# Optimization experiments

Hardware: AMD Instinct MI355X
Metric: run time of the kernel (lower is better)

Reference implementation:

```python
import jax, jax.numpy as jnp
import numpy as np

N = 50000
E = 800000
IN_DIM = 128
OUT_DIM = 128


def setup_inputs() -> dict:
    key = jax.random.key(0)
    k1, k2, k3, k4 = jax.random.split(key, 4)
    x = jax.random.normal(k1, (N, IN_DIM), dtype=jnp.float32)
    edge_index = jax.random.randint(k2, (2, E), 0, N, dtype=jnp.int64)
    # Linear(in_dim*2, out_dim) params
    W = jax.random.normal(k3, (2 * IN_DIM, OUT_DIM), dtype=jnp.float32) * (1.0 / np.sqrt(2 * IN_DIM))
    b = jax.random.normal(k4, (OUT_DIM,), dtype=jnp.float32) * 0.01
    return {"x": x, "edge_index": edge_index, "W": W, "b": b}


def reference(x, edge_index, W, b):
    src, dst = edge_index[0], edge_index[1]
    diff = x[src] - x[dst]                              # (E, C)
    # segment-max over destination nodes; empty segments get -inf identity
    seg_max = jax.ops.segment_max(diff, dst, num_segments=N)  # (N, C)
    counts = jax.ops.segment_sum(jnp.ones((E,), dtype=jnp.int32), dst, num_segments=N)
    # original code leaves zeros for nodes with no incoming edges
    max_diff = jnp.where((counts > 0)[:, None], seg_max, jnp.zeros_like(seg_max))
    x_cat = jnp.concatenate([x, max_diff], axis=-1)     # (N, 2C)
    return x_cat @ W + b
```

## Files before the change

kernel.cpp:

```cpp
#include <hip/hip_runtime.h>
#include <math.h>

#define NN 50000
#define NE 800000
#define CD 128
#define PB 3200
#define NBLK 1563
#define CSTR 1568
#define SCAP 160

typedef __attribute__((ext_vector_type(8))) short short8;
typedef __attribute__((ext_vector_type(4))) float f32x4;


__device__ inline unsigned pack2bf(float lo, float hi) {
    unsigned a = __float_as_uint(lo), b = __float_as_uint(hi);
    a = (a + 0x7fffu + ((a >> 16) & 1u)) >> 16;
    b = (b + 0x7fffu + ((b >> 16) & 1u)) & 0xffff0000u;
    return a | b;
}

__device__ inline unsigned short f2bf(float f) {
    unsigned u = __float_as_uint(f);
    return (unsigned short)((u + 0x7fffu + ((u >> 16) & 1u)) >> 16);
}

__device__ inline void fmax8(float* m, uint4 v) {
    m[0] = fmaxf(m[0], __uint_as_float(v.x << 16));
    m[1] = fmaxf(m[1], __uint_as_float(v.x & 0xffff0000u));
    m[2] = fmaxf(m[2], __uint_as_float(v.y << 16));
    m[3] = fmaxf(m[3], __uint_as_float(v.y & 0xffff0000u));
    m[4] = fmaxf(m[4], __uint_as_float(v.z << 16));
    m[5] = fmaxf(m[5], __uint_as_float(v.z & 0xffff0000u));
    m[6] = fmaxf(m[6], __uint_as_float(v.w << 16));
    m[7] = fmaxf(m[7], __uint_as_float(v.w & 0xffff0000u));
}


__global__ __launch_bounds__(256) void prep4_k(const int* __restrict__ ei,
                                               const float* __restrict__ x,
                                               const float* __restrict__ W,
                                               int* __restrict__ cur,
                                               int* __restrict__ ovfn,
                                               unsigned* __restrict__ ovf,
                                               unsigned* __restrict__ ent,
                                               unsigned* __restrict__ xb,
                                               unsigned short* __restrict__ wt) {
    int t = threadIdx.x;
    int b = blockIdx.x;
    int tid0 = b * 256 + t;
    int g = b & 7;
    int phase = (b >> 3) & 1;

    for (int p = 0; p < 2; p++) {
        if ((p ^ phase) == 0) {
            for (int e = tid0; e < NE; e += PB * 256) {
                int d = ei[NE + e];
                int s = ei[e];
                int bin = d >> 5;
                int pos = atomicAdd(&cur[g * CSTR + bin], 1);
                if (pos < SCAP) {
                    ent[(size_t)(g * NBLK + bin) * SCAP + pos] =
                        ((unsigned)s << 6) | (unsigned)(d & 31);
                } else {
                    int op = atomicAdd(ovfn, 1);
                    ovf[op] = ((unsigned)s << 16) | (unsigned)d;
                }
            }
        } else {
            for (int i = tid0; i < NN * CD / 4; i += PB * 256) {
                float4 v = ((const float4*)x)[i];
                uint2 r;
                r.x = pack2bf(v.x, v.y);
                r.y = pack2bf(v.z, v.w);
                ((uint2*)xb)[i] = r;
            }
        }
    }
    for (int i = tid0; i < 2 * CD * CD; i += PB * 256) {
        int n = i >> 8, k = i & 255;
        wt[(size_t)n * 256 + k] = f2bf(W[(size_t)k * 128 + n]);
    }
}


__global__ __launch_bounds__(256) void fused_k(const unsigned* __restrict__ xb,
                                               const int* __restrict__ cur,
                                               const int* __restrict__ ovfn,
                                               const unsigned* __restrict__ ovf,
                                               const unsigned* __restrict__ ent,
                                               const short* __restrict__ wt,
                                               const float* __restrict__ bias,
                                               float* __restrict__ out) {
    __shared__ unsigned short idx[32][72];
    __shared__ unsigned short amx[32][136];
    __shared__ int lcnt[32];
    __shared__ int spill[512];
    __shared__ int spn;

    int t = threadIdx.x;
    int b = blockIdx.x;
    int nbase = b * 32;

    if (t < 32) lcnt[t] = 0;
    if (t == 32) spn = 0;
    __syncthreads();

    for (int g = 0; g < 8; g++) {
        int cnt = min(cur[g * CSTR + b], SCAP);
        const unsigned* base = ent + (size_t)(g * NBLK + b) * SCAP;
        if (t < cnt) {
            unsigned w = base[t];
            int ln = (int)(w & 31u);
            int s = (int)(w >> 6);
            int pos = atomicAdd(&lcnt[ln], 1);
            if (pos < 64) idx[ln][pos] = (unsigned short)s;
            else { int sp = atomicAdd(&spn, 1); if (sp < 512) spill[sp] = (s << 6) | ln; }
        }
    }
    int ovN = min(ovfn[0], NE);
    for (int i = t; i < ovN; i += 256) {
        unsigned w = ovf[i];
        int d = (int)(w & 0xffffu);
        if ((d >> 5) == b) {
            int ln = d & 31;
            int s = (int)(w >> 16);
            int pos = atomicAdd(&lcnt[ln], 1);
            if (pos < 64) idx[ln][pos] = (unsigned short)s;
            else { int sp = atomicAdd(&spn, 1); if (sp < 512) spill[sp] = (s << 6) | ln; }
        }
    }
    __syncthreads();

    int w = t >> 6, lane = t & 63;
    int q = lane >> 4, c = lane & 15;
    int sN = min(spn, 512);
#pragma unroll 1
    for (int j = 0; j < 2; j++) {
        int ln = w * 8 + j * 4 + q;
        int node = nbase + ln;
        int cnt = lcnt[ln];
        int lim = min(cnt, 64);
        float m[8];
#pragma unroll
        for (int i = 0; i < 8; i++) m[i] = -INFINITY;

        for (int base = 0; base < lim; base += 8) {
            uint4 pk = *(const uint4*)&idx[ln][base];
            int s0 = (int)(pk.x & 0xffffu), s1 = (int)(pk.x >> 16);
            int s2 = (int)(pk.y & 0xffffu), s3 = (int)(pk.y >> 16);
            int s4 = (int)(pk.z & 0xffffu), s5 = (int)(pk.z >> 16);
            int s6 = (int)(pk.w & 0xffffu), s7 = (int)(pk.w >> 16);
            if (base + 8 <= lim) {
                fmax8(m, *(const uint4*)(xb + (size_t)s0 * 64 + c * 4));
                fmax8(m, *(const uint4*)(xb + (size_t)s1 * 64 + c * 4));
                fmax8(m, *(const uint4*)(xb + (size_t)s2 * 64 + c * 4));
                fmax8(m, *(const uint4*)(xb + (size_t)s3 * 64 + c * 4));
                fmax8(m, *(const uint4*)(xb + (size_t)s4 * 64 + c * 4));
                fmax8(m, *(const uint4*)(xb + (size_t)s5 * 64 + c * 4));
                fmax8(m, *(const uint4*)(xb + (size_t)s6 * 64 + c * 4));
                fmax8(m, *(const uint4*)(xb + (size_t)s7 * 64 + c * 4));
            } else {
                if (base + 0 < lim) fmax8(m, *(const uint4*)(xb + (size_t)s0 * 64 + c * 4));
                if (base + 1 < lim) fmax8(m, *(const uint4*)(xb + (size_t)s1 * 64 + c * 4));
                if (base + 2 < lim) fmax8(m, *(const uint4*)(xb + (size_t)s2 * 64 + c * 4));
                if (base + 3 < lim) fmax8(m, *(const uint4*)(xb + (size_t)s3 * 64 + c * 4));
                if (base + 4 < lim) fmax8(m, *(const uint4*)(xb + (size_t)s4 * 64 + c * 4));
                if (base + 5 < lim) fmax8(m, *(const uint4*)(xb + (size_t)s5 * 64 + c * 4));
                if (base + 6 < lim) fmax8(m, *(const uint4*)(xb + (size_t)s6 * 64 + c * 4));
                if (base + 7 < lim) fmax8(m, *(const uint4*)(xb + (size_t)s7 * 64 + c * 4));
            }
        }
        for (int i = 0; i < sN; i++) {
            int sw = spill[i];
            if ((sw & 63) == ln)
                fmax8(m, *(const uint4*)(xb + (size_t)(sw >> 6) * 64 + c * 4));
        }
        uint4 r = make_uint4(0u, 0u, 0u, 0u);
        if (cnt > 0) {
            uint4 xd = *(const uint4*)(xb + (size_t)node * 64 + c * 4);
            float d0 = m[0] - __uint_as_float(xd.x << 16);
            float d1 = m[1] - __uint_as_float(xd.x & 0xffff0000u);
            float d2 = m[2] - __uint_as_float(xd.y << 16);
            float d3 = m[3] - __uint_as_float(xd.y & 0xffff0000u);
            float d4 = m[4] - __uint_as_float(xd.z << 16);
            float d5 = m[5] - __uint_as_float(xd.z & 0xffff0000u);
            float d6 = m[6] - __uint_as_float(xd.w << 16);
            float d7 = m[7] - __uint_as_float(xd.w & 0xffff0000u);
            r.x = pack2bf(d0, d1);
            r.y = pack2bf(d2, d3);
            r.z = pack2bf(d4, d5);
            r.w = pack2bf(d6, d7);
        }
        *(uint4*)&amx[ln][c * 8] = r;
    }
    __syncthreads();

    int mm = lane & 15, g4 = lane >> 4;
    int rt = w & 1, ch = w >> 1;
    int r0 = nbase + rt * 16;
    int row = r0 + mm;
    bool rowok = row < NN;

    f32x4 acc[4];
#pragma unroll
    for (int ct = 0; ct < 4; ct++) {
        float bv = bias[ch * 64 + ct * 16 + mm];
        acc[ct] = (f32x4){bv, bv, bv, bv};
    }

    const short* xbs = (const short*)xb;
#pragma unroll
    for (int kc = 0; kc < 8; kc++) {
        int k0 = kc * 32;
        short8 a;
        if (kc < 4) {
            a = (short8){0, 0, 0, 0, 0, 0, 0, 0};
            if (rowok) a = *(const short8*)(xbs + (size_t)row * 128 + k0 + g4 * 8);
        } else {
            a = *(const short8*)&amx[rt * 16 + mm][(k0 - 128) + g4 * 8];
        }
#pragma unroll
        for (int ct = 0; ct < 4; ct++) {
            short8 bb = *(const short8*)(wt + (size_t)(ch * 64 + ct * 16 + mm) * 256 + k0 + g4 * 8);
            acc[ct] = __builtin_amdgcn_mfma_f32_16x16x32_bf16(a, bb, acc[ct], 0, 0, 0);
        }
    }

#pragma unroll
    for (int ct = 0; ct < 4; ct++) {
#pragma unroll
        for (int i = 0; i < 4; i++) {
            int rr = r0 + g4 * 4 + i;
            if (rr < NN) out[(size_t)rr * 128 + ch * 64 + ct * 16 + mm] = acc[ct][i];
        }
    }
}


extern "C" void kernel_launch(void* const* d_in, const int* in_sizes, int n_in,
                              void* d_out, int out_size, void* d_ws, size_t ws_size,
                              hipStream_t stream) {
    const float* x = (const float*)d_in[0];
    const int* ei = (const int*)d_in[1];
    const float* W = (const float*)d_in[2];
    const float* bias = (const float*)d_in[3];
    float* out = (float*)d_out;

    int* wsi = (int*)d_ws;
    int* cur   = wsi;
    int* ovfn  = wsi + 12544;
    unsigned* ovf = (unsigned*)(wsi + 12560);
    unsigned* ent = (unsigned*)(wsi + 812560);
    unsigned* xb  = (unsigned*)(wsi + 2813200);
    unsigned short* wt = (unsigned short*)(wsi + 6013200);

    hipMemsetAsync(cur, 0, (8 * CSTR + 16) * sizeof(int), stream);

    prep4_k<<<PB, 256, 0, stream>>>(ei, x, W, cur, ovfn, ovf, ent, xb, wt);
    fused_k<<<NBLK, 256, 0, stream>>>(xb, cur, ovfn, ovf, ent, (const short*)wt,
                                      bias, out);
}
```

Measured before the change: 193.1 us.

## Bucket edges into coarse 1024-node bins with block-local histograms

Edge binning now uses 49 coarse buckets of 1024 destination nodes. Each of 196 edge blocks first builds a shared-memory histogram and reserves space with one global atomic per bucket, which cuts global atomic contention sharply. The bf16 cast of x and W moves to a separate set of 2048 blocks. In exchange, each fused block must scan the whole bucket (about 16K entries) and filter for its own 32-node sub-bin, which multiplies entry reads by roughly 32x.

```diff
diff --git a/kernel.cpp b/kernel.cpp
--- a/kernel.cpp
+++ b/kernel.cpp
@@ -4,10 +4,12 @@
 #define NN 50000
 #define NE 800000
 #define CD 128
-#define PB 3200
-#define NBLK 1563
-#define CSTR 1568
-#define SCAP 160
+#define NBKT 49
+#define CAP 24576
+#define SLICE 4096
+#define EBLK 196
+#define CASTB 2048
+#define NBLK2 1563
 
 typedef __attribute__((ext_vector_type(8))) short short8;
 typedef __attribute__((ext_vector_type(4))) float f32x4;
@@ -37,49 +39,54 @@
 }
 
 
-__global__ __launch_bounds__(256) void prep4_k(const int* __restrict__ ei,
+__global__ __launch_bounds__(256) void prep5_k(const int* __restrict__ ei,
                                                const float* __restrict__ x,
                                                const float* __restrict__ W,
                                                int* __restrict__ cur,
                                                int* __restrict__ ovfn,
                                                unsigned* __restrict__ ovf,
-                                               unsigned* __restrict__ ent,
+                                               unsigned* __restrict__ csr,
                                                unsigned* __restrict__ xb,
                                                unsigned short* __restrict__ wt) {
+    int b = blockIdx.x;
     int t = threadIdx.x;
-    int b = blockIdx.x;
-    int tid0 = b * 256 + t;
-    int g = b & 7;
-    int phase = (b >> 3) & 1;
-
-    for (int p = 0; p < 2; p++) {
-        if ((p ^ phase) == 0) {
-            for (int e = tid0; e < NE; e += PB * 256) {
-                int d = ei[NE + e];
-                int s = ei[e];
-                int bin = d >> 5;
-                int pos = atomicAdd(&cur[g * CSTR + bin], 1);
-                if (pos < SCAP) {
-                    ent[(size_t)(g * NBLK + bin) * SCAP + pos] =
-                        ((unsigned)s << 6) | (unsigned)(d & 31);
-                } else {
-                    int op = atomicAdd(ovfn, 1);
-                    ovf[op] = ((unsigned)s << 16) | (unsigned)d;
-                }
+    if (b < EBLK) {
+        __shared__ int hist[64];
+        __shared__ int curs[64];
+        int e0 = b * SLICE;
+        int e1 = min(NE, e0 + SLICE);
+        if (t < 64) hist[t] = 0;
+        __syncthreads();
+        for (int e = e0 + t; e < e1; e += 256)
+            atomicAdd(&hist[((unsigned)ei[NE + e]) >> 10], 1);
+        __syncthreads();
+        if (t < NBKT) curs[t] = atomicAdd(&cur[t], hist[t]);
+        __syncthreads();
+        for (int e = e0 + t; e < e1; e += 256) {
+            int d = ei[NE + e];
+            int s = ei[e];
+            int bin = ((unsigned)d) >> 10;
+            int p = atomicAdd(&curs[bin], 1);
+            if (p < CAP) {
+                csr[(size_t)bin * CAP + p] = ((unsigned)s << 10) | (unsigned)(d & 1023);
+            } else {
+                int op = atomicAdd(ovfn, 1);
+                ovf[op] = ((unsigned)s << 16) | (unsigned)d;
             }
-        } else {
-            for (int i = tid0; i < NN * CD / 4; i += PB * 256) {
-                float4 v = ((const float4*)x)[i];
-                uint2 r;
-                r.x = pack2bf(v.x, v.y);
-                r.y = pack2bf(v.z, v.w);
-                ((uint2*)xb)[i] = r;
-            }
-        }
-    }
-    for (int i = tid0; i < 2 * CD * CD; i += PB * 256) {
-        int n = i >> 8, k = i & 255;
-        wt[(size_t)n * 256 + k] = f2bf(W[(size_t)k * 128 + n]);
+        }
+    } else {
+        int tid0 = (b - EBLK) * 256 + t;
+        for (int i = tid0; i < NN * CD / 4; i += CASTB * 256) {
+            float4 v = ((const float4*)x)[i];
+            uint2 r;
+            r.x = pack2bf(v.x, v.y);
+            r.y = pack2bf(v.z, v.w);
+            ((uint2*)xb)[i] = r;
+        }
+        for (int i = tid0; i < 2 * CD * CD; i += CASTB * 256) {
+            int n = i >> 8, k = i & 255;
+            wt[(size_t)n * 256 + k] = f2bf(W[(size_t)k * 128 + n]);
+        }
     }
 }
 
@@ -88,7 +95,7 @@
                                                const int* __restrict__ cur,
                                                const int* __restrict__ ovfn,
                                                const unsigned* __restrict__ ovf,
-                                               const unsigned* __restrict__ ent,
+                                               const unsigned* __restrict__ csr,
                                                const short* __restrict__ wt,
                                                const float* __restrict__ bias,
                                                float* __restrict__ out) {
@@ -99,20 +106,22 @@
     __shared__ int spn;
 
     int t = threadIdx.x;
-    int b = blockIdx.x;
-    int nbase = b * 32;
+    int B = blockIdx.x;
+    int qb = B >> 5;
+    int sub = B & 31;
+    int nbase = B * 32;
 
     if (t < 32) lcnt[t] = 0;
     if (t == 32) spn = 0;
     __syncthreads();
 
-    for (int g = 0; g < 8; g++) {
-        int cnt = min(cur[g * CSTR + b], SCAP);
-        const unsigned* base = ent + (size_t)(g * NBLK + b) * SCAP;
-        if (t < cnt) {
-            unsigned w = base[t];
+    int cnt = min(cur[qb], CAP);
+    const unsigned* base = csr + (size_t)qb * CAP;
+    for (int i = t; i < cnt; i += 256) {
+        unsigned w = base[i];
+        if ((int)((w >> 5) & 31) == sub) {
             int ln = (int)(w & 31u);
-            int s = (int)(w >> 6);
+            int s = (int)(w >> 10);
             int pos = atomicAdd(&lcnt[ln], 1);
             if (pos < 64) idx[ln][pos] = (unsigned short)s;
             else { int sp = atomicAdd(&spn, 1); if (sp < 512) spill[sp] = (s << 6) | ln; }
@@ -122,7 +131,7 @@
     for (int i = t; i < ovN; i += 256) {
         unsigned w = ovf[i];
         int d = (int)(w & 0xffffu);
-        if ((d >> 5) == b) {
+        if ((d >> 5) == B) {
             int ln = d & 31;
             int s = (int)(w >> 16);
             int pos = atomicAdd(&lcnt[ln], 1);
@@ -139,19 +148,19 @@
     for (int j = 0; j < 2; j++) {
         int ln = w * 8 + j * 4 + q;
         int node = nbase + ln;
-        int cnt = lcnt[ln];
-        int lim = min(cnt, 64);
+        int lc = lcnt[ln];
+        int lim = min(lc, 64);
         float m[8];
 #pragma unroll
         for (int i = 0; i < 8; i++) m[i] = -INFINITY;
 
-        for (int base = 0; base < lim; base += 8) {
-            uint4 pk = *(const uint4*)&idx[ln][base];
+        for (int bb = 0; bb < lim; bb += 8) {
+            uint4 pk = *(const uint4*)&idx[ln][bb];
             int s0 = (int)(pk.x & 0xffffu), s1 = (int)(pk.x >> 16);
             int s2 = (int)(pk.y & 0xffffu), s3 = (int)(pk.y >> 16);
             int s4 = (int)(pk.z & 0xffffu), s5 = (int)(pk.z >> 16);
             int s6 = (int)(pk.w & 0xffffu), s7 = (int)(pk.w >> 16);
-            if (base + 8 <= lim) {
+            if (bb + 8 <= lim) {
                 fmax8(m, *(const uint4*)(xb + (size_t)s0 * 64 + c * 4));
                 fmax8(m, *(const uint4*)(xb + (size_t)s1 * 64 + c * 4));
                 fmax8(m, *(const uint4*)(xb + (size_t)s2 * 64 + c * 4));
@@ -161,14 +170,14 @@
                 fmax8(m, *(const uint4*)(xb + (size_t)s6 * 64 + c * 4));
                 fmax8(m, *(const uint4*)(xb + (size_t)s7 * 64 + c * 4));
             } else {
-                if (base + 0 < lim) fmax8(m, *(const uint4*)(xb + (size_t)s0 * 64 + c * 4));
-                if (base + 1 < lim) fmax8(m, *(const uint4*)(xb + (size_t)s1 * 64 + c * 4));
-                if (base + 2 < lim) fmax8(m, *(const uint4*)(xb + (size_t)s2 * 64 + c * 4));
-                if (base + 3 < lim) fmax8(m, *(const uint4*)(xb + (size_t)s3 * 64 + c * 4));
-                if (base + 4 < lim) fmax8(m, *(const uint4*)(xb + (size_t)s4 * 64 + c * 4));
-                if (base + 5 < lim) fmax8(m, *(const uint4*)(xb + (size_t)s5 * 64 + c * 4));
-                if (base + 6 < lim) fmax8(m, *(const uint4*)(xb + (size_t)s6 * 64 + c * 4));
-                if (base + 7 < lim) fmax8(m, *(const uint4*)(xb + (size_t)s7 * 64 + c * 4));
+                if (bb + 0 < lim) fmax8(m, *(const uint4*)(xb + (size_t)s0 * 64 + c * 4));
+                if (bb + 1 < lim) fmax8(m, *(const uint4*)(xb + (size_t)s1 * 64 + c * 4));
+                if (bb + 2 < lim) fmax8(m, *(const uint4*)(xb + (size_t)s2 * 64 + c * 4));
+                if (bb + 3 < lim) fmax8(m, *(const uint4*)(xb + (size_t)s3 * 64 + c * 4));
+                if (bb + 4 < lim) fmax8(m, *(const uint4*)(xb + (size_t)s4 * 64 + c * 4));
+                if (bb + 5 < lim) fmax8(m, *(const uint4*)(xb + (size_t)s5 * 64 + c * 4));
+                if (bb + 6 < lim) fmax8(m, *(const uint4*)(xb + (size_t)s6 * 64 + c * 4));
+                if (bb + 7 < lim) fmax8(m, *(const uint4*)(xb + (size_t)s7 * 64 + c * 4));
             }
         }
         for (int i = 0; i < sN; i++) {
@@ -177,7 +186,7 @@
                 fmax8(m, *(const uint4*)(xb + (size_t)(sw >> 6) * 64 + c * 4));
         }
         uint4 r = make_uint4(0u, 0u, 0u, 0u);
-        if (cnt > 0) {
+        if (lc > 0) {
             uint4 xd = *(const uint4*)(xb + (size_t)node * 64 + c * 4);
             float d0 = m[0] - __uint_as_float(xd.x << 16);
             float d1 = m[1] - __uint_as_float(xd.x & 0xffff0000u);
@@ -249,15 +258,15 @@
 
     int* wsi = (int*)d_ws;
     int* cur   = wsi;
-    int* ovfn  = wsi + 12544;
-    unsigned* ovf = (unsigned*)(wsi + 12560);
-    unsigned* ent = (unsigned*)(wsi + 812560);
-    unsigned* xb  = (unsigned*)(wsi + 2813200);
-    unsigned short* wt = (unsigned short*)(wsi + 6013200);
-
-    hipMemsetAsync(cur, 0, (8 * CSTR + 16) * sizeof(int), stream);
-
-    prep4_k<<<PB, 256, 0, stream>>>(ei, x, W, cur, ovfn, ovf, ent, xb, wt);
-    fused_k<<<NBLK, 256, 0, stream>>>(xb, cur, ovfn, ovf, ent, (const short*)wt,
-                                      bias, out);
-}
+    int* ovfn  = wsi + 64;
+    unsigned* ovf = (unsigned*)(wsi + 80);
+    unsigned* csr = (unsigned*)(wsi + 800080);
+    unsigned* xb  = (unsigned*)(wsi + 2004304);
+    unsigned short* wt = (unsigned short*)(wsi + 5204304);
+
+    hipMemsetAsync(cur, 0, 80 * sizeof(int), stream);
+
+    prep5_k<<<EBLK + CASTB, 256, 0, stream>>>(ei, x, W, cur, ovfn, ovf, csr, xb, wt);
+    fused_k<<<NBLK2, 256, 0, stream>>>(xb, cur, ovfn, ovf, csr, (const short*)wt,
+                                       bias, out);
+}
```

New measurement: 200.8 us. 1.04x slower.
